# Performance work log

Measured on AMD Instinct MI355X. Metric: run time of the kernel, lower is better.

Reference implementation:

```python
import jax, jax.numpy as jnp
import numpy as np

N = 50000
IN_DIM = 128
HID = 64
HEADS = 4
OUT_DIM = 2
NEG_SLOPE = 0.2


def setup_inputs() -> dict:
    key = jax.random.key(0)
    ks = jax.random.split(key, 10)
    x = jax.random.normal(ks[0], (N, IN_DIM), dtype=jnp.float32)
    edge_index = jax.random.randint(ks[1], (2, 800000), 0, N, dtype=jnp.int64)
    s = 0.1
    W1 = jax.random.normal(ks[2], (IN_DIM, HEADS * HID), dtype=jnp.float32) * s
    att_src1 = jax.random.normal(ks[3], (HEADS, HID), dtype=jnp.float32) * s
    att_dst1 = jax.random.normal(ks[4], (HEADS, HID), dtype=jnp.float32) * s
    b1 = jnp.zeros((HEADS * HID,), dtype=jnp.float32)
    W2 = jax.random.normal(ks[5], (HEADS * HID, 1 * OUT_DIM), dtype=jnp.float32) * s
    att_src2 = jax.random.normal(ks[6], (1, OUT_DIM), dtype=jnp.float32) * s
    att_dst2 = jax.random.normal(ks[7], (1, OUT_DIM), dtype=jnp.float32) * s
    b2 = jnp.zeros((OUT_DIM,), dtype=jnp.float32)
    return {"x": x, "edge_index": edge_index, "W1": W1, "att_src1": att_src1,
            "att_dst1": att_dst1, "b1": b1, "W2": W2, "att_src2": att_src2,
            "att_dst2": att_dst2, "b2": b2}


def gat_conv(x, W, att_src, att_dst, b, src, dst, heads, ch):
    # x: [N, F_in] -> h: [N, H, C]
    n = x.shape[0]
    h = (x @ W).reshape(n, heads, ch)
    a_s = jnp.einsum('nhc,hc->nh', h, att_src)  # [N, H]
    a_d = jnp.einsum('nhc,hc->nh', h, att_dst)  # [N, H]
    e = jax.nn.leaky_relu(a_s[src] + a_d[dst], NEG_SLOPE)  # [E, H]
    # segment softmax over incoming edges of each destination node
    m = jax.ops.segment_max(e, dst, num_segments=n)
    ex = jnp.exp(e - m[dst])
    z = jax.ops.segment_sum(ex, dst, num_segments=n)
    alpha = ex / z[dst]  # [E, H]
    msg = h[src] * alpha[:, :, None]  # [E, H, C]
    out = jax.ops.segment_sum(msg, dst, num_segments=n)  # [N, H, C]
    return out.reshape(n, heads * ch) + b


def reference(x, edge_index, W1, att_src1, att_dst1, b1, W2, att_src2, att_dst2, b2):
    n = x.shape[0]
    loop = jnp.arange(n, dtype=edge_index.dtype)
    src = jnp.concatenate([edge_index[0], loop])  # add_self_loops (PyG default)
    dst = jnp.concatenate([edge_index[1], loop])
    h = gat_conv(x, W1, att_src1, att_dst1, b1, src, dst, HEADS, HID)
    h = jax.nn.elu(h)
    # dropout is identity at inference
    out = gat_conv(h, W2, att_src2, att_dst2, b2, src, dst, 1, OUT_DIM)
    return out
```

## Files before the change

kernel.cpp:

```cpp
#include <hip/hip_runtime.h>

#define NN     50000
#define E_RAW  800000
#define ETOT   (E_RAW + NN)
#define FIN    128
#define FH     256
#define NEG    0.2f
#define BCAP   64

#define P_PART 8
#define DPW    6250
#define R_REP  32
#define EPW    (E_RAW / R_REP)
#define CNT_WGS (P_PART * R_REP)
#define PREP_WGS 8
#define OFF_NB  ((NN + 255) / 256)
#define GEMM_NB ((NN + 63) / 64)

typedef __attribute__((ext_vector_type(8))) short s16x8;
typedef __attribute__((ext_vector_type(4))) float f32x4;

static __device__ __forceinline__ float leaky(float v) { return v > 0.f ? v : NEG * v; }

static __device__ __forceinline__ unsigned short f2bf(float f) {
    unsigned u = __float_as_uint(f);
    unsigned r = u + 0x7fffu + ((u >> 16) & 1u);
    return (unsigned short)(r >> 16);
}

__global__ __launch_bounds__(1024) void k_count(const int* __restrict__ ei,
                                                const float* __restrict__ W1,
                                                unsigned short* __restrict__ Wt_bf,
                                                int* __restrict__ pcnt)
{
    const int t = threadIdx.x;
    if (blockIdx.x >= CNT_WGS) {
        const int base = (blockIdx.x - CNT_WGS) * 4096;
        for (int i = t; i < 4096; i += 1024) {
            int idx = base + i;
            int k = idx >> 8, col = idx & 255;
            Wt_bf[col * FIN + k] = f2bf(W1[k * FH + col]);
        }
        return;
    }
    __shared__ int lcnt[DPW];
    const int p  = blockIdx.x >> 5;
    const int r  = blockIdx.x & 31;
    const int lo = p * DPW;
    for (int i = t; i < DPW; i += 1024) lcnt[i] = 0;
    __syncthreads();
    const int ebase = r * EPW, eend = ebase + EPW;
    for (int e0 = ebase + t * 4; e0 < eend; e0 += 4096) {
        int4 dv4 = *(const int4*)&ei[E_RAW + e0];
#pragma unroll
        for (int k = 0; k < 4; k++) {
            unsigned rel = (unsigned)((&dv4.x)[k] - lo);
            if (rel < DPW) atomicAdd(&lcnt[rel], 1);
        }
    }
    __syncthreads();
    for (int i = t; i < DPW; i += 1024)
        pcnt[r * NN + lo + i] = lcnt[i];
}

__global__ __launch_bounds__(256) void k_gx(const float* __restrict__ x,
                                            const unsigned short* __restrict__ Wt_bf,
                                            const float* __restrict__ att_src,
                                            const float* __restrict__ att_dst,
                                            const int* __restrict__ pcnt,
                                            int* __restrict__ soff,
                                            int* __restrict__ cnt,
                                            int* __restrict__ csr_src,
                                            unsigned short* __restrict__ h1b,
                                            float* __restrict__ a_s,
                                            float* __restrict__ a_d)
{
    const int t = threadIdx.x;
    if (blockIdx.x < OFF_NB) {
        int d = blockIdx.x * 256 + t;
        if (d >= NN) return;
        int run = 1;
#pragma unroll
        for (int r = 0; r < R_REP; r++) {
            soff[r * NN + d] = run;
            run += pcnt[r * NN + d];
        }
        cnt[d] = run;
        csr_src[(size_t)d << 6] = d;
        return;
    }

    __shared__ unsigned short Sbuf[64 * 256];
    const int w    = t >> 6;
    const int lane = t & 63;
    const int li   = lane & 15;
    const int q8   = (lane >> 4) * 8;
    const int quad = lane >> 4;
    const int n0   = (blockIdx.x - OFF_NB) * 64;

    {
        const int node_l = t >> 2;
        const int k0 = (t & 3) * 32;
        int nn = n0 + node_l; if (nn >= NN) nn = NN - 1;
        const float* xp = &x[(size_t)nn * FIN + k0];
        unsigned short* xd = &Sbuf[node_l * 136 + k0];
#pragma unroll
        for (int i = 0; i < 8; i++) {
            float4 v = *(const float4*)&xp[i * 4];
            xd[i * 4 + 0] = f2bf(v.x);
            xd[i * 4 + 1] = f2bf(v.y);
            xd[i * 4 + 2] = f2bf(v.z);
            xd[i * 4 + 3] = f2bf(v.w);
        }
    }
    __syncthreads();

    f32x4 acc[4][4];
#pragma unroll
    for (int i = 0; i < 4; i++)
#pragma unroll
        for (int j = 0; j < 4; j++) acc[i][j] = (f32x4){0.f, 0.f, 0.f, 0.f};

#pragma unroll
    for (int kki = 0; kki < 4; kki++) {
        const int kk = kki * 32;
        s16x8 af[4], bf[4];
#pragma unroll
        for (int n16 = 0; n16 < 4; n16++) {
            int col = w * 64 + n16 * 16 + li;
            bf[n16] = *(const s16x8*)&Wt_bf[col * FIN + kk + q8];
        }
#pragma unroll
        for (int m16 = 0; m16 < 4; m16++)
            af[m16] = *(const s16x8*)&Sbuf[(m16 * 16 + li) * 136 + kk + q8];
#pragma unroll
        for (int m16 = 0; m16 < 4; m16++)
#pragma unroll
            for (int n16 = 0; n16 < 4; n16++)
                acc[m16][n16] = __builtin_amdgcn_mfma_f32_16x16x32_bf16(
                    af[m16], bf[n16], acc[m16][n16], 0, 0, 0);
    }

    {
        float as_c[4], ad_c[4];
#pragma unroll
        for (int n16 = 0; n16 < 4; n16++) {
            int col = w * 64 + n16 * 16 + li;
            as_c[n16] = att_src[col];
            ad_c[n16] = att_dst[col];
        }
#pragma unroll
        for (int m16 = 0; m16 < 4; m16++) {
            float ps[4], pd[4];
#pragma unroll
            for (int reg = 0; reg < 4; reg++) {
                float s = 0.f, d = 0.f;
#pragma unroll
                for (int n16 = 0; n16 < 4; n16++) {
                    s += acc[m16][n16][reg] * as_c[n16];
                    d += acc[m16][n16][reg] * ad_c[n16];
                }
                ps[reg] = s; pd[reg] = d;
            }
#pragma unroll
            for (int off = 1; off < 16; off <<= 1) {
#pragma unroll
                for (int reg = 0; reg < 4; reg++) {
                    ps[reg] += __shfl_xor(ps[reg], off);
                    pd[reg] += __shfl_xor(pd[reg], off);
                }
            }
            if (li == 0) {
#pragma unroll
                for (int reg = 0; reg < 4; reg++) {
                    int node = n0 + m16 * 16 + quad * 4 + reg;
                    if (node < NN) {
                        a_s[node * 4 + w] = ps[reg];
                        a_d[node * 4 + w] = pd[reg];
                    }
                }
            }
        }
    }

    __syncthreads();
#pragma unroll
    for (int m16 = 0; m16 < 4; m16++)
#pragma unroll
        for (int n16 = 0; n16 < 4; n16++)
#pragma unroll
            for (int reg = 0; reg < 4; reg++)
                Sbuf[(m16 * 16 + quad * 4 + reg) * FH + w * 64 + n16 * 16 + li] =
                    f2bf(acc[m16][n16][reg]);
    __syncthreads();
    {
        const int node_l = t >> 2;
        const int c0 = (t & 3) * 64;
        int node = n0 + node_l;
        if (node < NN) {
#pragma unroll
            for (int i = 0; i < 8; i++)
                *(uint4*)&h1b[(size_t)node * FH + c0 + i * 8] =
                    *(const uint4*)&Sbuf[node_l * FH + c0 + i * 8];
        }
    }
}

__global__ __launch_bounds__(1024) void k_scat2(const int* __restrict__ ei,
                                                const int* __restrict__ soff,
                                                int* __restrict__ csr_src)
{
    __shared__ int cur[DPW];
    const int t  = threadIdx.x;
    const int p  = blockIdx.x >> 5;
    const int r  = blockIdx.x & 31;
    const int lo = p * DPW;
    for (int i = t; i < DPW; i += 1024)
        cur[i] = soff[r * NN + lo + i];
    __syncthreads();
    const int ebase = r * EPW, eend = ebase + EPW;
    for (int e0 = ebase + t * 4; e0 < eend; e0 += 4096) {
        int4 sv4 = *(const int4*)&ei[e0];
        int4 dv4 = *(const int4*)&ei[E_RAW + e0];
#pragma unroll
        for (int k = 0; k < 4; k++) {
            int d = (&dv4.x)[k];
            unsigned rel = (unsigned)(d - lo);
            if (rel < DPW) {
                int pos = atomicAdd(&cur[rel], 1);
                if (pos < BCAP)
                    csr_src[((size_t)d << 6) + pos] = (&sv4.x)[k];
            }
        }
    }
}

__global__ __launch_bounds__(256) void k_agg1(const int* __restrict__ cnt,
                                              const int* __restrict__ csr_src,
                                              const float* __restrict__ a_s1,
                                              const float* __restrict__ a_d1,
                                              const unsigned short* __restrict__ h1b,
                                              const float* __restrict__ b1,
                                              const float* __restrict__ W2,
                                              const float* __restrict__ att_src2,
                                              const float* __restrict__ att_dst2,
                                              float4* __restrict__ nd4)
{
    const int t    = threadIdx.x;
    const int lane = t & 63;
    const int sl   = lane & 15;
    const int n    = blockIdx.x * 16 + (t >> 4);
    int m = cnt[n]; if (m > BCAP) m = BCAP;
    const int h  = sl >> 2;
    const int c0 = sl << 4;
    const float ad_h = a_d1[n * 4 + h];
    const int* sp = &csr_src[(size_t)n << 6];

    int mmax = m;
    mmax = max(mmax, __shfl_xor(mmax, 16));
    mmax = max(mmax, __shfl_xor(mmax, 32));

    float acc[16];
#pragma unroll
    for (int i = 0; i < 16; i++) acc[i] = 0.f;
    float z = 0.f;

    int sv = sp[sl];
    for (int jb = 0; jb < mmax; jb += 16) {
        int svn = 0;
        if (jb + 16 < mmax) svn = sp[sl + jb + 16];
        int lim = mmax - jb; if (lim > 16) lim = 16;
        for (int j4 = 0; j4 < lim; j4 += 4) {
#pragma unroll
            for (int u = 0; u < 4; u++) {
                const int jj = j4 + u;
                const int j  = jb + jj;
                int s = __shfl(sv, (lane & 48) + jj);
                const bool live = j < m;
                s = live ? s : 0;
                float ex = __expf(leaky(a_s1[s * 4 + h] + ad_h));
                ex = live ? ex : 0.f;
                const unsigned short* hp = h1b + ((size_t)s << 8) + c0;
                uint4 r0 = *(const uint4*)hp;
                uint4 r1 = *(const uint4*)(hp + 8);
                acc[0]  += __uint_as_float(r0.x << 16)         * ex;
                acc[1]  += __uint_as_float(r0.x & 0xffff0000u) * ex;
                acc[2]  += __uint_as_float(r0.y << 16)         * ex;
                acc[3]  += __uint_as_float(r0.y & 0xffff0000u) * ex;
                acc[4]  += __uint_as_float(r0.z << 16)         * ex;
                acc[5]  += __uint_as_float(r0.z & 0xffff0000u) * ex;
                acc[6]  += __uint_as_float(r0.w << 16)         * ex;
                acc[7]  += __uint_as_float(r0.w & 0xffff0000u) * ex;
                acc[8]  += __uint_as_float(r1.x << 16)         * ex;
                acc[9]  += __uint_as_float(r1.x & 0xffff0000u) * ex;
                acc[10] += __uint_as_float(r1.y << 16)         * ex;
                acc[11] += __uint_as_float(r1.y & 0xffff0000u) * ex;
                acc[12] += __uint_as_float(r1.z << 16)         * ex;
                acc[13] += __uint_as_float(r1.z & 0xffff0000u) * ex;
                acc[14] += __uint_as_float(r1.w << 16)         * ex;
                acc[15] += __uint_as_float(r1.w & 0xffff0000u) * ex;
                z += ex;
            }
        }
        sv = svn;
    }

    const float rz = 1.0f / z;
    float s0 = 0.f, s1 = 0.f;
#pragma unroll
    for (int i = 0; i < 16; i += 4) {
        float4 bb = *(const float4*)&b1[c0 + i];
        float v0 = acc[i]     * rz + bb.x;
        float v1 = acc[i + 1] * rz + bb.y;
        float v2 = acc[i + 2] * rz + bb.z;
        float v3 = acc[i + 3] * rz + bb.w;
        v0 = v0 > 0.f ? v0 : __expf(v0) - 1.f;
        v1 = v1 > 0.f ? v1 : __expf(v1) - 1.f;
        v2 = v2 > 0.f ? v2 : __expf(v2) - 1.f;
        v3 = v3 > 0.f ? v3 : __expf(v3) - 1.f;
        float4 wa = *(const float4*)&W2[(c0 + i) * 2];
        float4 wb = *(const float4*)&W2[(c0 + i) * 2 + 4];
        s0 += v0 * wa.x + v1 * wa.z + v2 * wb.x + v3 * wb.z;
        s1 += v0 * wa.y + v1 * wa.w + v2 * wb.y + v3 * wb.w;
    }
#pragma unroll
    for (int off = 1; off < 16; off <<= 1) {
        s0 += __shfl_xor(s0, off);
        s1 += __shfl_xor(s1, off);
    }
    if (sl == 0) {
        float4 nd;
        nd.x = s0; nd.y = s1;
        nd.z = s0 * att_src2[0] + s1 * att_src2[1];
        nd.w = s0 * att_dst2[0] + s1 * att_dst2[1];
        nd4[n] = nd;
    }
}

__global__ __launch_bounds__(256) void k_agg2(const int* __restrict__ cnt,
                                              const int* __restrict__ csr_src,
                                              const float4* __restrict__ nd4,
                                              const float* __restrict__ b2,
                                              float* __restrict__ out)
{
    const int l = threadIdx.x & 15;
    const int n = blockIdx.x * 16 + (threadIdx.x >> 4);
    if (n >= NN) return;
    int m = cnt[n]; if (m > BCAP) m = BCAP;
    const int* sp = &csr_src[(size_t)n << 6];
    const float ad = nd4[n].w;
    float z = 0.f, a0 = 0.f, a1 = 0.f;
    for (int j = l; j < m; j += 16) {
        int s = sp[j];
        float4 f = nd4[s];
        float ex = __expf(leaky(f.z + ad));
        z  += ex;
        a0 += f.x * ex;
        a1 += f.y * ex;
    }
#pragma unroll
    for (int off = 8; off; off >>= 1) {
        z  += __shfl_xor(z, off);
        a0 += __shfl_xor(a0, off);
        a1 += __shfl_xor(a1, off);
    }
    if (l == 0) {
        out[n * 2 + 0] = a0 / z + b2[0];
        out[n * 2 + 1] = a1 / z + b2[1];
    }
}

extern "C" void kernel_launch(void* const* d_in, const int* in_sizes, int n_in,
                              void* d_out, int out_size, void* d_ws, size_t ws_size,
                              hipStream_t stream)
{
    const float* x        = (const float*)d_in[0];
    const int*   ei       = (const int*)d_in[1];
    const float* W1       = (const float*)d_in[2];
    const float* att_src1 = (const float*)d_in[3];
    const float* att_dst1 = (const float*)d_in[4];
    const float* b1       = (const float*)d_in[5];
    const float* W2       = (const float*)d_in[6];
    const float* att_src2 = (const float*)d_in[7];
    const float* att_dst2 = (const float*)d_in[8];
    const float* b2       = (const float*)d_in[9];
    float* out = (float*)d_out;

    int*    csr_src = (int*)d_ws;
    unsigned short* h1b = (unsigned short*)(csr_src + (size_t)NN * 64);
    unsigned short* Wt_bf = h1b + (size_t)NN * FH;
    int*    pcnt  = (int*)(Wt_bf + FH * FIN);
    int*    soff  = pcnt + (size_t)NN * R_REP;
    int*    cnt   = soff + (size_t)NN * R_REP;
    float*  a_s1  = (float*)(cnt + NN);
    float*  a_d1  = a_s1 + (size_t)NN * 4;
    float4* nd4   = (float4*)(a_d1 + (size_t)NN * 4);

    k_count<<<CNT_WGS + PREP_WGS, 1024, 0, stream>>>(ei, W1, Wt_bf, pcnt);
    k_gx<<<OFF_NB + GEMM_NB, 256, 0, stream>>>(x, Wt_bf, att_src1, att_dst1,
                                               pcnt, soff, cnt, csr_src,
                                               h1b, a_s1, a_d1);
    k_scat2<<<CNT_WGS, 1024, 0, stream>>>(ei, soff, csr_src);
    k_agg1<<<NN / 16, 256, 0, stream>>>(cnt, csr_src, a_s1, a_d1, h1b,
                                        b1, W2, att_src2, att_dst2, nd4);
    k_agg2<<<(NN + 15) / 16, 256, 0, stream>>>(cnt, csr_src, nd4, b2, out);
}
```

Baseline: 212.7 us.

## Split agg1 feature halves across blocks and parallelize edges within each wave

Each wave in the layer-1 aggregation now handles one destination node and one half of the 256 features. Its four 16-lane groups take different edges in parallel, then reduce the partial sums with cross-lane shuffles. Each half writes a partial 2-wide projection, and agg2 adds the two halves and computes the layer-2 attention logits itself. The aim is more parallelism and memory-level parallelism per node, with fewer serial edge iterations. The cost is twice as many blocks, reading a_s1 and the neighbour list twice, and extra shuffles and loads in agg2.

```diff
diff --git a/kernel.cpp b/kernel.cpp
--- a/kernel.cpp
+++ b/kernel.cpp
@@ -16,6 +16,7 @@
 #define PREP_WGS 8
 #define OFF_NB  ((NN + 255) / 256)
 #define GEMM_NB ((NN + 63) / 64)
+#define AGG1_NB 25000
 
 typedef __attribute__((ext_vector_type(8))) short s16x8;
 typedef __attribute__((ext_vector_type(4))) float f32x4;
@@ -242,73 +243,62 @@
                                               const unsigned short* __restrict__ h1b,
                                               const float* __restrict__ b1,
                                               const float* __restrict__ W2,
-                                              const float* __restrict__ att_src2,
-                                              const float* __restrict__ att_dst2,
-                                              float4* __restrict__ nd4)
+                                              float2* __restrict__ ndp)
 {
     const int t    = threadIdx.x;
     const int lane = t & 63;
     const int sl   = lane & 15;
-    const int n    = blockIdx.x * 16 + (t >> 4);
+    const int u    = lane >> 4;
+    const int r8   = blockIdx.x & 7;
+    const int half = r8 >> 2;
+    const int g    = (blockIdx.x >> 3) * 4 + (r8 & 3);
+    const int n    = g * 4 + (t >> 6);
+
     int m = cnt[n]; if (m > BCAP) m = BCAP;
-    const int h  = sl >> 2;
-    const int c0 = sl << 4;
+    const int c0 = half * 128 + sl * 8;
+    const int h  = c0 >> 6;
     const float ad_h = a_d1[n * 4 + h];
     const int* sp = &csr_src[(size_t)n << 6];
 
-    int mmax = m;
-    mmax = max(mmax, __shfl_xor(mmax, 16));
-    mmax = max(mmax, __shfl_xor(mmax, 32));
-
-    float acc[16];
-#pragma unroll
-    for (int i = 0; i < 16; i++) acc[i] = 0.f;
+    int sv = 0;
+    if (lane < m) sv = sp[lane];
+
+    float acc[8];
+#pragma unroll
+    for (int i = 0; i < 8; i++) acc[i] = 0.f;
     float z = 0.f;
 
-    int sv = sp[sl];
-    for (int jb = 0; jb < mmax; jb += 16) {
-        int svn = 0;
-        if (jb + 16 < mmax) svn = sp[sl + jb + 16];
-        int lim = mmax - jb; if (lim > 16) lim = 16;
-        for (int j4 = 0; j4 < lim; j4 += 4) {
-#pragma unroll
-            for (int u = 0; u < 4; u++) {
-                const int jj = j4 + u;
-                const int j  = jb + jj;
-                int s = __shfl(sv, (lane & 48) + jj);
-                const bool live = j < m;
-                s = live ? s : 0;
-                float ex = __expf(leaky(a_s1[s * 4 + h] + ad_h));
-                ex = live ? ex : 0.f;
-                const unsigned short* hp = h1b + ((size_t)s << 8) + c0;
-                uint4 r0 = *(const uint4*)hp;
-                uint4 r1 = *(const uint4*)(hp + 8);
-                acc[0]  += __uint_as_float(r0.x << 16)         * ex;
-                acc[1]  += __uint_as_float(r0.x & 0xffff0000u) * ex;
-                acc[2]  += __uint_as_float(r0.y << 16)         * ex;
-                acc[3]  += __uint_as_float(r0.y & 0xffff0000u) * ex;
-                acc[4]  += __uint_as_float(r0.z << 16)         * ex;
-                acc[5]  += __uint_as_float(r0.z & 0xffff0000u) * ex;
-                acc[6]  += __uint_as_float(r0.w << 16)         * ex;
-                acc[7]  += __uint_as_float(r0.w & 0xffff0000u) * ex;
-                acc[8]  += __uint_as_float(r1.x << 16)         * ex;
-                acc[9]  += __uint_as_float(r1.x & 0xffff0000u) * ex;
-                acc[10] += __uint_as_float(r1.y << 16)         * ex;
-                acc[11] += __uint_as_float(r1.y & 0xffff0000u) * ex;
-                acc[12] += __uint_as_float(r1.z << 16)         * ex;
-                acc[13] += __uint_as_float(r1.z & 0xffff0000u) * ex;
-                acc[14] += __uint_as_float(r1.w << 16)         * ex;
-                acc[15] += __uint_as_float(r1.w & 0xffff0000u) * ex;
-                z += ex;
-            }
-        }
-        sv = svn;
+    for (int j4 = 0; j4 < m; j4 += 4) {
+        const int j = j4 + u;
+        const bool live = j < m;
+        int s = __shfl(sv, j & 63);
+        s = live ? s : 0;
+        float ex = __expf(leaky(a_s1[s * 4 + h] + ad_h));
+        ex = live ? ex : 0.f;
+        const unsigned short* hp = h1b + ((size_t)s << 8) + c0;
+        uint4 r0 = *(const uint4*)hp;
+        acc[0] += __uint_as_float(r0.x << 16)         * ex;
+        acc[1] += __uint_as_float(r0.x & 0xffff0000u) * ex;
+        acc[2] += __uint_as_float(r0.y << 16)         * ex;
+        acc[3] += __uint_as_float(r0.y & 0xffff0000u) * ex;
+        acc[4] += __uint_as_float(r0.z << 16)         * ex;
+        acc[5] += __uint_as_float(r0.z & 0xffff0000u) * ex;
+        acc[6] += __uint_as_float(r0.w << 16)         * ex;
+        acc[7] += __uint_as_float(r0.w & 0xffff0000u) * ex;
+        z += ex;
+    }
+
+#pragma unroll
+    for (int off = 16; off < 64; off <<= 1) {
+#pragma unroll
+        for (int i = 0; i < 8; i++) acc[i] += __shfl_xor(acc[i], off);
+        z += __shfl_xor(z, off);
     }
 
     const float rz = 1.0f / z;
     float s0 = 0.f, s1 = 0.f;
 #pragma unroll
-    for (int i = 0; i < 16; i += 4) {
+    for (int i = 0; i < 8; i += 4) {
         float4 bb = *(const float4*)&b1[c0 + i];
         float v0 = acc[i]     * rz + bb.x;
         float v1 = acc[i + 1] * rz + bb.y;
@@ -328,18 +318,15 @@
         s0 += __shfl_xor(s0, off);
         s1 += __shfl_xor(s1, off);
     }
-    if (sl == 0) {
-        float4 nd;
-        nd.x = s0; nd.y = s1;
-        nd.z = s0 * att_src2[0] + s1 * att_src2[1];
-        nd.w = s0 * att_dst2[0] + s1 * att_dst2[1];
-        nd4[n] = nd;
-    }
+    if (lane == 0)
+        ndp[(size_t)half * NN + n] = make_float2(s0, s1);
 }
 
 __global__ __launch_bounds__(256) void k_agg2(const int* __restrict__ cnt,
                                               const int* __restrict__ csr_src,
-                                              const float4* __restrict__ nd4,
+                                              const float2* __restrict__ ndp,
+                                              const float* __restrict__ att_src2,
+                                              const float* __restrict__ att_dst2,
                                               const float* __restrict__ b2,
                                               float* __restrict__ out)
 {
@@ -348,15 +335,18 @@
     if (n >= NN) return;
     int m = cnt[n]; if (m > BCAP) m = BCAP;
     const int* sp = &csr_src[(size_t)n << 6];
-    const float ad = nd4[n].w;
+    const float as0 = att_src2[0], as1 = att_src2[1];
+    float2 o0 = ndp[n], o1 = ndp[NN + n];
+    const float ad = (o0.x + o1.x) * att_dst2[0] + (o0.y + o1.y) * att_dst2[1];
     float z = 0.f, a0 = 0.f, a1 = 0.f;
     for (int j = l; j < m; j += 16) {
         int s = sp[j];
-        float4 f = nd4[s];
-        float ex = __expf(leaky(f.z + ad));
+        float2 f0 = ndp[s], f1 = ndp[NN + s];
+        float sx = f0.x + f1.x, sy = f0.y + f1.y;
+        float ex = __expf(leaky(sx * as0 + sy * as1 + ad));
         z  += ex;
-        a0 += f.x * ex;
-        a1 += f.y * ex;
+        a0 += sx * ex;
+        a1 += sy * ex;
     }
 #pragma unroll
     for (int off = 8; off; off >>= 1) {
@@ -394,14 +384,15 @@
     int*    cnt   = soff + (size_t)NN * R_REP;
     float*  a_s1  = (float*)(cnt + NN);
     float*  a_d1  = a_s1 + (size_t)NN * 4;
-    float4* nd4   = (float4*)(a_d1 + (size_t)NN * 4);
+    float2* ndp   = (float2*)(a_d1 + (size_t)NN * 4);
 
     k_count<<<CNT_WGS + PREP_WGS, 1024, 0, stream>>>(ei, W1, Wt_bf, pcnt);
     k_gx<<<OFF_NB + GEMM_NB, 256, 0, stream>>>(x, Wt_bf, att_src1, att_dst1,
                                                pcnt, soff, cnt, csr_src,
                                                h1b, a_s1, a_d1);
     k_scat2<<<CNT_WGS, 1024, 0, stream>>>(ei, soff, csr_src);
-    k_agg1<<<NN / 16, 256, 0, stream>>>(cnt, csr_src, a_s1, a_d1, h1b,
-                                        b1, W2, att_src2, att_dst2, nd4);
-    k_agg2<<<(NN + 15) / 16, 256, 0, stream>>>(cnt, csr_src, nd4, b2, out);
-}
+    k_agg1<<<AGG1_NB, 256, 0, stream>>>(cnt, csr_src, a_s1, a_d1, h1b,
+                                        b1, W2, ndp);
+    k_agg2<<<(NN + 15) / 16, 256, 0, stream>>>(cnt, csr_src, ndp,
+                                               att_src2, att_dst2, b2, out);
+}
```

Result: no change. 209.4 us (-1.6%).
